# Performance work log

Measured on AMD Instinct MI355X. Metric: run time of the kernel, lower is better.

Reference implementation:

```python
import jax, jax.numpy as jnp
import numpy as np

HID = 2048      # hidden_size
H = 16          # num_heads == num_kv_heads (stack in fwd forces MHA)
DH = HID // H   # head_size = 128
QKV = 3 * H * DH  # 6144
THETA = 10000.0
EPS = 1e-5      # flash-attn RMSNorm default eps
B, L = 4, 2048


def setup_inputs() -> dict:
    key = jax.random.key(0)
    k1, k2, k3 = jax.random.split(key, 3)
    hidden_states = jax.random.normal(k1, (B, L, HID), dtype=jnp.float32)
    # weights stored as (in, out); scaled like a typical init so activations stay sane
    W_qkvg = jax.random.normal(k2, (HID, QKV + HID), dtype=jnp.float32) * 0.02
    W_out = jax.random.normal(k3, (HID, HID), dtype=jnp.float32) * 0.02
    return {"hidden_states": hidden_states, "W_qkvg": W_qkvg, "W_out": W_out}


def _rmsnorm(x):
    # elementwise_affine=False: pure rms normalization over head dim
    return x * jax.lax.rsqrt(jnp.mean(x * x, axis=-1, keepdims=True) + EPS)


def _rope(x, seqlen_offset=0):
    # x: (B, L, H, DH), non-interleaved (GPT-NeoX style rotate-half)
    half = DH // 2
    inv_freq = 1.0 / (THETA ** (jnp.arange(half, dtype=jnp.float32) * 2.0 / DH))
    pos = jnp.arange(seqlen_offset, seqlen_offset + x.shape[1], dtype=jnp.float32)
    ang = pos[:, None] * inv_freq[None, :]                  # (L, half)
    cos = jnp.cos(ang)[None, :, None, :]                    # (1,L,1,half)
    sin = jnp.sin(ang)[None, :, None, :]
    x1, x2 = x[..., :half], x[..., half:]
    return jnp.concatenate([x1 * cos - x2 * sin, x1 * sin + x2 * cos], axis=-1)


def _attention_forward(hidden_states, W_qkvg, W_out):
    b, l, _ = hidden_states.shape
    proj = hidden_states @ W_qkvg                           # (B,L,QKV+HID)
    qkv_flat, gate = proj[..., :QKV], proj[..., QKV:]
    gate = jax.nn.sigmoid(gate)
    qkv = qkv_flat.reshape(b, l, 3 * H, DH)
    q, k, v = qkv[:, :, :H], qkv[:, :, H:2 * H], qkv[:, :, 2 * H:]
    q = _rope(_rmsnorm(q))
    k = _rope(_rmsnorm(k))
    # causal softmax attention (math of flash_attn_func)
    scores = jnp.einsum('blhd,bmhd->bhlm', q, k) / np.sqrt(DH).astype(np.float32)
    causal = jnp.tril(jnp.ones((l, l), dtype=bool))
    scores = jnp.where(causal[None, None], scores, jnp.finfo(scores.dtype).min)
    attn = jax.nn.softmax(scores, axis=-1)
    out = jnp.einsum('bhlm,bmhd->blhd', attn, v).reshape(b, l, HID)
    out = out * gate
    return out @ W_out


def reference(hidden_states, W_qkvg, W_out):
    return _attention_forward(hidden_states, W_qkvg, W_out)
```

## Files before the change

### kernel.cpp

```cpp
#include <hip/hip_runtime.h>


typedef __attribute__((ext_vector_type(8))) short bf16x8;
typedef __attribute__((ext_vector_type(4))) float f32x4;
typedef __attribute__((ext_vector_type(4))) unsigned short us4;

#if __has_builtin(__builtin_amdgcn_exp2f)
#define EXP2(x) __builtin_amdgcn_exp2f(x)
#else
#define EXP2(x) exp2f(x)
#endif

__device__ __forceinline__ unsigned short f2bf(float f) {
    unsigned int x = __float_as_uint(f);
    unsigned int r = x + 0x7fffu + ((x >> 16) & 1u);
    return (unsigned short)(r >> 16);
}
__device__ __forceinline__ unsigned short f2bf_fast(float f) {
    return (unsigned short)((__float_as_uint(f) + 0x8000u) >> 16);
}
__device__ __forceinline__ float bf2f(unsigned short u) {
    return __uint_as_float(((unsigned int)u) << 16);
}

__device__ __forceinline__ void gll16(const unsigned short* g, unsigned short* l) {
    __builtin_amdgcn_global_load_lds(
        (const __attribute__((address_space(1))) unsigned int*)g,
        (__attribute__((address_space(3))) unsigned int*)l, 16, 0, 0);
}

__device__ __forceinline__ void barx() {
    asm volatile("" ::: "memory");
    __builtin_amdgcn_s_barrier();
    asm volatile("" ::: "memory");
}
#define LGKM0() asm volatile("s_waitcnt lgkmcnt(0)" ::: "memory")
#define VM6()   asm volatile("s_waitcnt vmcnt(6)" ::: "memory")
#define VM0()   asm volatile("s_waitcnt vmcnt(0)" ::: "memory")

__global__ __launch_bounds__(256) void cvt_bf16(const float* __restrict__ in,
                                                unsigned short* __restrict__ out) {
    int i = blockIdx.x * 256 + threadIdx.x;
    float4 v = ((const float4*)in)[i];
    us4 r;
    r[0] = f2bf(v.x); r[1] = f2bf(v.y); r[2] = f2bf(v.z); r[3] = f2bf(v.w);
    ((us4*)out)[i] = r;
}

__global__ __launch_bounds__(256) void transpose_cvt(const float* __restrict__ in,
                                                     unsigned short* __restrict__ out,
                                                     int R, int C) {
    __shared__ float t[32][33];
    int c0 = blockIdx.x * 32, r0 = blockIdx.y * 32;
    int tx = threadIdx.x, ty = threadIdx.y;
#pragma unroll
    for (int i = 0; i < 4; i++)
        t[ty + i * 8][tx] = in[(size_t)(r0 + ty + i * 8) * C + c0 + tx];
    __syncthreads();
#pragma unroll
    for (int i = 0; i < 4; i++)
        out[(size_t)(c0 + ty + i * 8) * R + r0 + tx] = f2bf(t[tx][ty + i * 8]);
}

__device__ __forceinline__ void gemm256_core(const unsigned short* __restrict__ A,
                                             const unsigned short* __restrict__ Bt,
                                             int K, int rowA0, int colB0,
                                             unsigned short* sm,
                                             f32x4 acc[8][4]) {
    const int tid = threadIdx.x;
    const int w = tid >> 6, lane = tid & 63;
    const int quad = lane >> 4, l15 = lane & 15;
    const int wm = w >> 2, wn = w & 3;
    const int lr = lane >> 3;
    const int lc = ((lane & 7) ^ lr) * 8;
    const int NT = K >> 6;

    const unsigned short* pA = A  + (size_t)(rowA0 + w * 16 + lr) * K + lc;
    const unsigned short* pB = Bt + (size_t)(colB0 + w * 16 + lr) * K + lc;
    unsigned short* lw = sm + w * 16 * 64;

#define STAGE(tt, isB, h)                                                       \
    do {                                                                        \
        const unsigned short* gp_ = ((isB) ? pB : pA) +                         \
            (size_t)(h) * 128 * K + (size_t)(tt) * 64;                          \
        unsigned short* lp_ = lw + (((tt) & 1) * 4 + (isB) * 2 + (h)) * 8192;   \
        gll16(gp_, lp_);                                                        \
        gll16(gp_ + (size_t)8 * K, lp_ + 8 * 64);                               \
    } while (0)

    STAGE(0, 1, 0); STAGE(0, 1, 1); STAGE(0, 0, 0); STAGE(0, 0, 1);
    STAGE(1, 1, 0); STAGE(1, 1, 1); STAGE(1, 0, 0);
    VM6();
    barx();

    for (int t = 0; t < NT; ++t) {
        const unsigned short* Asl = sm + ((t & 1) * 4 + wm) * 8192;
        const unsigned short* Bsl = sm + ((t & 1) * 4 + 2 + (wn >> 1)) * 8192;
        bf16x8 bfrag[4][2];
#pragma unroll
        for (int q = 0; q < 4; ++q) {
            if (q == 0) {
#pragma unroll
                for (int nj = 0; nj < 4; ++nj)
#pragma unroll
                    for (int kk = 0; kk < 2; ++kk) {
                        int r = (wn & 1) * 64 + nj * 16 + l15;
                        bfrag[nj][kk] = *(const bf16x8*)&Bsl[r * 64 +
                            (((kk * 4 + quad) ^ (r & 7)) * 8)];
                    }
            }
            bf16x8 afr[2][2];
#pragma unroll
            for (int mi = 0; mi < 2; ++mi)
#pragma unroll
                for (int kk = 0; kk < 2; ++kk) {
                    int r = q * 32 + mi * 16 + l15;
                    afr[mi][kk] = *(const bf16x8*)&Asl[r * 64 +
                        (((kk * 4 + quad) ^ (r & 7)) * 8)];
                }
            if (q == 0)      { if (t + 1 < NT) STAGE(t + 1, 0, 1); }
            else if (q == 1) { if (t + 2 < NT) STAGE(t + 2, 1, 0); }
            else if (q == 2) { if (t + 2 < NT) STAGE(t + 2, 1, 1); }
            else {
                if (t + 2 < NT)      { STAGE(t + 2, 0, 0); VM6(); }
                else if (t + 1 < NT) { VM0(); }
            }
            barx();
            LGKM0();
            __builtin_amdgcn_s_setprio(1);
#pragma unroll
            for (int mi = 0; mi < 2; ++mi)
#pragma unroll
                for (int nj = 0; nj < 4; ++nj)
#pragma unroll
                    for (int kk = 0; kk < 2; ++kk)
                        acc[q * 2 + mi][nj] = __builtin_amdgcn_mfma_f32_16x16x32_bf16(
                            afr[mi][kk], bfrag[nj][kk], acc[q * 2 + mi][nj], 0, 0, 0);
            __builtin_amdgcn_s_setprio(0);
            barx();
        }
    }
#undef STAGE
}

__global__ __launch_bounds__(512) void gemm_qkvg(const unsigned short* __restrict__ A,
                                                 const unsigned short* __restrict__ Bt,
                                                 unsigned short* __restrict__ Qb,
                                                 unsigned short* __restrict__ Kb,
                                                 unsigned short* __restrict__ Vt,
                                                 unsigned short* __restrict__ Gb) {
    __shared__ unsigned short sm[8 * 8192];
    f32x4 acc[8][4];
    f32x4 z = {0.f, 0.f, 0.f, 0.f};
#pragma unroll
    for (int i = 0; i < 8; i++)
#pragma unroll
        for (int j = 0; j < 4; j++) acc[i][j] = z;

    const int g = blockIdx.y * 32 + blockIdx.x;
    const int gs = (g & 7) * 128 + (g >> 3);
    const int bx = gs & 31, by = gs >> 5;
    const int rowA0 = by * 256, colB0 = bx * 256;
    gemm256_core(A, Bt, 2048, rowA0, colB0, sm, acc);

    const int tid = threadIdx.x, w = tid >> 6, lane = tid & 63;
    const int quad = lane >> 4, l15 = lane & 15;
    const int wm = w >> 2, wn = w & 3;
    const int sec = colB0 >> 11;
    const int hbase = (colB0 & 2047) >> 7;

    if (sec == 2) {
#pragma unroll
        for (int mi = 0; mi < 8; ++mi)
#pragma unroll
            for (int nj = 0; nj < 4; ++nj)
#pragma unroll
                for (int i = 0; i < 4; ++i) {
                    int ll = wm * 128 + mi * 16 + quad * 4 + i;
                    int c  = wn * 64 + nj * 16 + l15;
                    int hh = c >> 7, d = c & 127;
                    sm[hh * 32768 + d * 256 + (((ll >> 3) ^ (d & 31)) * 8) + (ll & 7)] =
                        f2bf(acc[mi][nj][i]);
                }
        __syncthreads();
        const int b_ = rowA0 >> 11, l0 = rowA0 & 2047;
        const int d = tid >> 2, part = tid & 3;
#pragma unroll
        for (int hh = 0; hh < 2; ++hh) {
            unsigned short* drow = Vt +
                ((size_t)(b_ * 16 + hbase + hh) * 128 + d) * 2048 + l0 + part * 64;
#pragma unroll
            for (int j = 0; j < 8; ++j) {
                int chunk = part * 8 + j;
                *(bf16x8*)(drow + j * 8) =
                    *(const bf16x8*)&sm[hh * 32768 + d * 256 + ((chunk ^ (d & 31)) * 8)];
            }
        }
    } else if (sec == 3) {
#pragma unroll
        for (int mi = 0; mi < 8; ++mi)
#pragma unroll
            for (int nj = 0; nj < 4; ++nj)
#pragma unroll
                for (int i = 0; i < 4; ++i) {
                    int rowg = rowA0 + wm * 128 + mi * 16 + quad * 4 + i;
                    int c = wn * 64 + nj * 16 + l15;
                    int h = hbase + (c >> 7), d = c & 127;
                    float gv = 1.f / (1.f + __expf(-acc[mi][nj][i]));
                    Gb[((size_t)rowg << 11) + h * 128 + d] = f2bf(gv);
                }
    } else {
        unsigned short* dst = (sec == 0) ? Qb : Kb;
#pragma unroll
        for (int mi = 0; mi < 8; ++mi)
#pragma unroll
            for (int nj = 0; nj < 4; ++nj)
#pragma unroll
                for (int i = 0; i < 4; ++i) {
                    int rowg = rowA0 + wm * 128 + mi * 16 + quad * 4 + i;
                    int c = wn * 64 + nj * 16 + l15;
                    int h = hbase + (c >> 7), d = c & 127;
                    int b_ = rowg >> 11, l_ = rowg & 2047;
                    dst[(((size_t)(b_ * 16 + h) * 2048 + l_) << 7) + d] =
                        f2bf(acc[mi][nj][i]);
                }
    }
}

__global__ __launch_bounds__(512) void gemm_out(const unsigned short* __restrict__ A,
                                                const unsigned short* __restrict__ Bt,
                                                float* __restrict__ C) {
    __shared__ unsigned short sm[8 * 8192];
    f32x4 acc[8][4];
    f32x4 z = {0.f, 0.f, 0.f, 0.f};
#pragma unroll
    for (int i = 0; i < 8; i++)
#pragma unroll
        for (int j = 0; j < 4; j++) acc[i][j] = z;

    const int g = blockIdx.y * 8 + blockIdx.x;
    const int gs = (g & 7) * 32 + (g >> 3);
    const int bx = gs & 7, by = gs >> 3;
    const int rowA0 = by * 256, colB0 = bx * 256;
    gemm256_core(A, Bt, 2048, rowA0, colB0, sm, acc);

    const int tid = threadIdx.x, w = tid >> 6, lane = tid & 63;
    const int quad = lane >> 4, l15 = lane & 15;
    const int wm = w >> 2, wn = w & 3;
#pragma unroll
    for (int mi = 0; mi < 8; ++mi)
#pragma unroll
        for (int nj = 0; nj < 4; ++nj)
#pragma unroll
            for (int i = 0; i < 4; ++i) {
                int rowg = rowA0 + wm * 128 + mi * 16 + quad * 4 + i;
                int col = colB0 + wn * 64 + nj * 16 + l15;
                C[(size_t)rowg * 2048 + col] = acc[mi][nj][i];
            }
}

__global__ __launch_bounds__(256) void rmsnorm_rope(unsigned short* __restrict__ Qp,
                                                    unsigned short* __restrict__ Kp) {
    unsigned short* X = blockIdx.y ? Kp : Qp;
    const int tid = threadIdx.x;
    const int row = blockIdx.x * 4 + (tid >> 6);
    const int lane = tid & 63;
    unsigned short* p = X + (size_t)row * 128;
    const int l_ = row & 2047;
    float x1 = bf2f(p[lane]);
    float x2 = bf2f(p[lane + 64]);
    float ss = x1 * x1 + x2 * x2;
#pragma unroll
    for (int off = 32; off >= 1; off >>= 1) ss += __shfl_xor(ss, off, 64);
    float r = rsqrtf(ss * (1.f / 128.f) + 1e-5f);
    x1 *= r; x2 *= r;
    float inv = exp2f(-(float)lane * (13.287712379549449f / 64.f));
    float ang = (float)l_ * inv;
    float sn, cs;
    sincosf(ang, &sn, &cs);
    p[lane]      = f2bf(x1 * cs - x2 * sn);
    p[lane + 64] = f2bf(x1 * sn + x2 * cs);
}

__global__ __launch_bounds__(512) void fa_kernel(const unsigned short* __restrict__ Q,
                                                 const unsigned short* __restrict__ K,
                                                 const unsigned short* __restrict__ Vt,
                                                 const unsigned short* __restrict__ G,
                                                 unsigned short* __restrict__ Og) {
    __shared__ unsigned short Ks[64 * 128];
    __shared__ unsigned short Vs[128 * 64];
    __shared__ unsigned short Ps[256 * 32];
    const int g = blockIdx.x;
    const int bh = (g & 7) | ((g >> 6) << 3);
    const int qc = (g >> 3) & 7;
    const int tid = threadIdx.x, w = tid >> 6, lane = tid & 63;
    const int quad = lane >> 4, l15 = lane & 15;
    const int sw = l15 & 7;
    const int qrow0 = qc * 256 + w * 32;
    const float CS = 0.12751740395609812f;

    bf16x8 qf[2][4];
#pragma unroll
    for (int mi = 0; mi < 2; mi++)
#pragma unroll
        for (int kt = 0; kt < 4; kt++)
            qf[mi][kt] = *(const bf16x8*)(Q + ((size_t)bh * 2048 + qrow0 + mi * 16 + l15) * 128
                                             + kt * 32 + quad * 8);

    f32x4 o[2][8];
    f32x4 z = {0.f, 0.f, 0.f, 0.f};
#pragma unroll
    for (int mi = 0; mi < 2; mi++)
#pragma unroll
        for (int nj = 0; nj < 8; nj++) o[mi][nj] = z;
    float rowsum[2][4];
#pragma unroll
    for (int mi = 0; mi < 2; mi++)
#pragma unroll
        for (int i = 0; i < 4; i++) rowsum[mi][i] = 0.f;

    const unsigned short* Kbase = K + (size_t)bh * 2048 * 128;
    const unsigned short* Vtb   = Vt + (size_t)bh * 128 * 2048;

    const int pr0 = w * 32 + l15, pr1 = pr0 + 16;
    const int pk0 = (pr0 >> 1) & 3, pk1 = (pr1 >> 1) & 3;

    const int NJ = 4 * (qc + 1);
    for (int j = 0; j < NJ; j++) {
        __syncthreads();

        {
            const int rowoff = lane >> 4, c = lane & 15;
#pragma unroll
            for (int i = 0; i < 2; i++) {
                int r0 = w * 8 + i * 4;
                int row = r0 + rowoff;
                int cs_ = (c & 8) | ((c & 7) ^ (row & 7));
                gll16(Kbase + (size_t)(j * 64 + row) * 128 + cs_ * 8, Ks + r0 * 128);
            }
        }
        {
            const int rowoff = lane >> 3, c = lane & 7;
#pragma unroll
            for (int i = 0; i < 2; i++) {
                int r0 = w * 16 + i * 8;
                int row = r0 + rowoff;
                gll16(Vtb + (size_t)row * 2048 + j * 64 + ((c ^ (row & 7)) * 8),
                      Vs + r0 * 64);
            }
        }
        __syncthreads();

        if (j * 64 >= qrow0 + 32) continue;

        f32x4 s[2][4];
#pragma unroll
        for (int mi = 0; mi < 2; mi++)
#pragma unroll
            for (int nj = 0; nj < 4; nj++) s[mi][nj] = z;
#pragma unroll
        for (int kt = 0; kt < 4; kt++)
#pragma unroll
            for (int nj = 0; nj < 4; nj++) {
                bf16x8 bfr = *(const bf16x8*)&Ks[(nj * 16 + l15) * 128 +
                                                 (((kt * 4 + quad) ^ sw) * 8)];
                s[0][nj] = __builtin_amdgcn_mfma_f32_16x16x32_bf16(qf[0][kt], bfr, s[0][nj], 0, 0, 0);
                s[1][nj] = __builtin_amdgcn_mfma_f32_16x16x32_bf16(qf[1][kt], bfr, s[1][nj], 0, 0, 0);
            }

        const bool diag = (j * 64 + 63 > qrow0);
#pragma unroll
        for (int hh = 0; hh < 2; hh++) {
#pragma unroll
            for (int mi = 0; mi < 2; mi++)
#pragma unroll
                for (int njh = 0; njh < 2; njh++) {
                    const int nj = hh * 2 + njh;
#pragma unroll
                    for (int i = 0; i < 4; i++) {
                        float pp = EXP2(s[mi][nj][i] * CS);
                        int row_l = mi * 16 + quad * 4 + i;
                        if (diag) {
                            int col_g = j * 64 + nj * 16 + l15;
                            if (col_g > qrow0 + row_l) pp = 0.f;
                        }
                        rowsum[mi][i] += pp;
                        int row = w * 32 + row_l;
                        int kv = njh * 16 + l15;
                        Ps[row * 32 + ((((kv >> 3) ^ ((row >> 1) & 3)) * 8)) + (kv & 7)] =
                            f2bf_fast(pp);
                    }
                }
            bf16x8 a0 = *(const bf16x8*)&Ps[pr0 * 32 + ((quad ^ pk0) * 8)];
            bf16x8 a1 = *(const bf16x8*)&Ps[pr1 * 32 + ((quad ^ pk1) * 8)];
#pragma unroll
            for (int nj = 0; nj < 8; nj++) {
                bf16x8 bfr = *(const bf16x8*)&Vs[(nj * 16 + l15) * 64 +
                                                 (((hh * 4 + quad) ^ sw) * 8)];
                o[0][nj] = __builtin_amdgcn_mfma_f32_16x16x32_bf16(a0, bfr, o[0][nj], 0, 0, 0);
                o[1][nj] = __builtin_amdgcn_mfma_f32_16x16x32_bf16(a1, bfr, o[1][nj], 0, 0, 0);
            }
        }
    }

    const int b_ = bh >> 4, h = bh & 15;
#pragma unroll
    for (int mi = 0; mi < 2; mi++)
#pragma unroll
        for (int i = 0; i < 4; i++) {
            float t = rowsum[mi][i];
#pragma unroll
            for (int off = 1; off < 16; off <<= 1) t += __shfl_xor(t, off, 16);
            float rl = 1.f / t;
            int l_ = qrow0 + mi * 16 + quad * 4 + i;
#pragma unroll
            for (int nj = 0; nj < 8; nj++) {
                int d = nj * 16 + l15;
                size_t gi = ((size_t)(b_ * 2048 + l_) * 2048) + h * 128 + d;
                Og[gi] = f2bf(o[mi][nj][i] * rl * bf2f(G[gi]));
            }
        }
}

extern "C" void kernel_launch(void* const* d_in, const int* in_sizes, int n_in,
                              void* d_out, int out_size, void* d_ws, size_t ws_size,
                              hipStream_t stream) {
    const float* X  = (const float*)d_in[0];
    const float* Wq = (const float*)d_in[1];
    const float* Wo = (const float*)d_in[2];
    float* out = (float*)d_out;

    char* ws = (char*)d_ws;
    const size_t SZ = 33554432ull;
    unsigned short* Xb  = (unsigned short*)(ws);
    unsigned short* Wqt = (unsigned short*)(ws + SZ);
    unsigned short* Wot = (unsigned short*)(ws + 2 * SZ);
    unsigned short* Qb  = (unsigned short*)(ws + 2 * SZ + 8388608ull);
    unsigned short* Kb  = (unsigned short*)(ws + 3 * SZ + 8388608ull);
    unsigned short* Vt  = (unsigned short*)(ws + 4 * SZ + 8388608ull);
    unsigned short* Gb  = (unsigned short*)(ws + 5 * SZ + 8388608ull);
    unsigned short* OG  = Xb;

    cvt_bf16<<<16384, 256, 0, stream>>>(X, Xb);
    transpose_cvt<<<dim3(256, 64), dim3(32, 8), 0, stream>>>(Wq, Wqt, 2048, 8192);
    transpose_cvt<<<dim3(64, 64),  dim3(32, 8), 0, stream>>>(Wo, Wot, 2048, 2048);

    gemm_qkvg<<<dim3(32, 32), 512, 0, stream>>>(Xb, Wqt, Qb, Kb, Vt, Gb);

    rmsnorm_rope<<<dim3(32768, 2), 256, 0, stream>>>(Qb, Kb);

    fa_kernel<<<512, 512, 0, stream>>>(Qb, Kb, Vt, Gb, OG);

    gemm_out<<<dim3(8, 32), 512, 0, stream>>>(OG, Wot, out);
}
```

Measured before the change: 702.7 us.

## Double-buffer K/V tiles in flash attention and remap QKVG GEMM block order

The attention kernel now keeps two LDS buffers for K and V. It issues the async global-to-LDS loads for the next tile before computing the current one, waiting with vmcnt(4) instead of a full drain, so load latency can overlap the MFMA and softmax work. Separately, the QKVG GEMM changes how block ids map to tiles: each XCD gets groups of four adjacent column tiles, which is meant to improve L2 reuse of B. The cost is double the K/V LDS footprint, which may reduce occupancy.

```diff
diff --git a/kernel.cpp b/kernel.cpp
--- a/kernel.cpp
+++ b/kernel.cpp
@@ -36,6 +36,7 @@
 }
 #define LGKM0() asm volatile("s_waitcnt lgkmcnt(0)" ::: "memory")
 #define VM6()   asm volatile("s_waitcnt vmcnt(6)" ::: "memory")
+#define VM4()   asm volatile("s_waitcnt vmcnt(4)" ::: "memory")
 #define VM0()   asm volatile("s_waitcnt vmcnt(0)" ::: "memory")
 
 __global__ __launch_bounds__(256) void cvt_bf16(const float* __restrict__ in,
@@ -158,8 +159,8 @@
         for (int j = 0; j < 4; j++) acc[i][j] = z;
 
     const int g = blockIdx.y * 32 + blockIdx.x;
-    const int gs = (g & 7) * 128 + (g >> 3);
-    const int bx = gs & 31, by = gs >> 5;
+    const int xcd = g & 7, lo = g >> 3;
+    const int bx = xcd * 4 + (lo & 3), by = lo >> 2;
     const int rowA0 = by * 256, colB0 = bx * 256;
     gemm256_core(A, Bt, 2048, rowA0, colB0, sm, acc);
 
@@ -287,8 +288,8 @@
                                                  const unsigned short* __restrict__ Vt,
                                                  const unsigned short* __restrict__ G,
                                                  unsigned short* __restrict__ Og) {
-    __shared__ unsigned short Ks[64 * 128];
-    __shared__ unsigned short Vs[128 * 64];
+    __shared__ unsigned short Ks[2][64 * 128];
+    __shared__ unsigned short Vs[2][128 * 64];
     __shared__ unsigned short Ps[256 * 32];
     const int g = blockIdx.x;
     const int bh = (g & 7) | ((g >> 6) << 3);
@@ -322,86 +323,94 @@
     const unsigned short* Kbase = K + (size_t)bh * 2048 * 128;
     const unsigned short* Vtb   = Vt + (size_t)bh * 128 * 2048;
 
+    const int krow = lane >> 4, kc = lane & 15;
+    const int vrow = lane >> 3, vc = lane & 7;
+
+#define STAGE_KV(jj, buf)                                                        \
+    do {                                                                         \
+        _Pragma("unroll")                                                        \
+        for (int i_ = 0; i_ < 2; i_++) {                                         \
+            int r0_ = w * 8 + i_ * 4;                                            \
+            int row_ = r0_ + krow;                                               \
+            int cs_ = (kc & 8) | ((kc & 7) ^ (row_ & 7));                        \
+            gll16(Kbase + (size_t)((jj) * 64 + row_) * 128 + cs_ * 8,            \
+                  &Ks[buf][r0_ * 128]);                                          \
+        }                                                                        \
+        _Pragma("unroll")                                                        \
+        for (int i_ = 0; i_ < 2; i_++) {                                         \
+            int r0_ = w * 16 + i_ * 8;                                           \
+            int row_ = r0_ + vrow;                                               \
+            gll16(Vtb + (size_t)row_ * 2048 + (jj) * 64 + ((vc ^ (row_ & 7)) * 8), \
+                  &Vs[buf][r0_ * 64]);                                           \
+        }                                                                        \
+    } while (0)
+
     const int pr0 = w * 32 + l15, pr1 = pr0 + 16;
     const int pk0 = (pr0 >> 1) & 3, pk1 = (pr1 >> 1) & 3;
 
     const int NJ = 4 * (qc + 1);
+
+    STAGE_KV(0, 0);
+
     for (int j = 0; j < NJ; j++) {
-        __syncthreads();
-
-        {
-            const int rowoff = lane >> 4, c = lane & 15;
-#pragma unroll
-            for (int i = 0; i < 2; i++) {
-                int r0 = w * 8 + i * 4;
-                int row = r0 + rowoff;
-                int cs_ = (c & 8) | ((c & 7) ^ (row & 7));
-                gll16(Kbase + (size_t)(j * 64 + row) * 128 + cs_ * 8, Ks + r0 * 128);
+        const int cur = j & 1;
+        if (j + 1 < NJ) { STAGE_KV(j + 1, cur ^ 1); VM4(); }
+        else            { VM0(); }
+        barx();
+
+        if (j * 64 < qrow0 + 32) {
+            f32x4 s[2][4];
+#pragma unroll
+            for (int mi = 0; mi < 2; mi++)
+#pragma unroll
+                for (int nj = 0; nj < 4; nj++) s[mi][nj] = z;
+#pragma unroll
+            for (int kt = 0; kt < 4; kt++)
+#pragma unroll
+                for (int nj = 0; nj < 4; nj++) {
+                    bf16x8 bfr = *(const bf16x8*)&Ks[cur][(nj * 16 + l15) * 128 +
+                                                         (((kt * 4 + quad) ^ sw) * 8)];
+                    s[0][nj] = __builtin_amdgcn_mfma_f32_16x16x32_bf16(qf[0][kt], bfr, s[0][nj], 0, 0, 0);
+                    s[1][nj] = __builtin_amdgcn_mfma_f32_16x16x32_bf16(qf[1][kt], bfr, s[1][nj], 0, 0, 0);
+                }
+
+            const bool diag = (j * 64 + 63 > qrow0);
+#pragma unroll
+            for (int hh = 0; hh < 2; hh++) {
+#pragma unroll
+                for (int mi = 0; mi < 2; mi++)
+#pragma unroll
+                    for (int njh = 0; njh < 2; njh++) {
+                        const int nj = hh * 2 + njh;
+#pragma unroll
+                        for (int i = 0; i < 4; i++) {
+                            float pp = EXP2(s[mi][nj][i] * CS);
+                            int row_l = mi * 16 + quad * 4 + i;
+                            if (diag) {
+                                int col_g = j * 64 + nj * 16 + l15;
+                                if (col_g > qrow0 + row_l) pp = 0.f;
+                            }
+                            rowsum[mi][i] += pp;
+                            int row = w * 32 + row_l;
+                            int kv = njh * 16 + l15;
+                            Ps[row * 32 + ((((kv >> 3) ^ ((row >> 1) & 3)) * 8)) + (kv & 7)] =
+                                f2bf_fast(pp);
+                        }
+                    }
+                bf16x8 a0 = *(const bf16x8*)&Ps[pr0 * 32 + ((quad ^ pk0) * 8)];
+                bf16x8 a1 = *(const bf16x8*)&Ps[pr1 * 32 + ((quad ^ pk1) * 8)];
+#pragma unroll
+                for (int nj = 0; nj < 8; nj++) {
+                    bf16x8 bfr = *(const bf16x8*)&Vs[cur][(nj * 16 + l15) * 64 +
+                                                          (((hh * 4 + quad) ^ sw) * 8)];
+                    o[0][nj] = __builtin_amdgcn_mfma_f32_16x16x32_bf16(a0, bfr, o[0][nj], 0, 0, 0);
+                    o[1][nj] = __builtin_amdgcn_mfma_f32_16x16x32_bf16(a1, bfr, o[1][nj], 0, 0, 0);
+                }
             }
         }
-        {
-            const int rowoff = lane >> 3, c = lane & 7;
-#pragma unroll
-            for (int i = 0; i < 2; i++) {
-                int r0 = w * 16 + i * 8;
-                int row = r0 + rowoff;
-                gll16(Vtb + (size_t)row * 2048 + j * 64 + ((c ^ (row & 7)) * 8),
-                      Vs + r0 * 64);
-            }
-        }
-        __syncthreads();
-
-        if (j * 64 >= qrow0 + 32) continue;
-
-        f32x4 s[2][4];
-#pragma unroll
-        for (int mi = 0; mi < 2; mi++)
-#pragma unroll
-            for (int nj = 0; nj < 4; nj++) s[mi][nj] = z;
-#pragma unroll
-        for (int kt = 0; kt < 4; kt++)
-#pragma unroll
-            for (int nj = 0; nj < 4; nj++) {
-                bf16x8 bfr = *(const bf16x8*)&Ks[(nj * 16 + l15) * 128 +
-                                                 (((kt * 4 + quad) ^ sw) * 8)];
-                s[0][nj] = __builtin_amdgcn_mfma_f32_16x16x32_bf16(qf[0][kt], bfr, s[0][nj], 0, 0, 0);
-                s[1][nj] = __builtin_amdgcn_mfma_f32_16x16x32_bf16(qf[1][kt], bfr, s[1][nj], 0, 0, 0);
-            }
-
-        const bool diag = (j * 64 + 63 > qrow0);
-#pragma unroll
-        for (int hh = 0; hh < 2; hh++) {
-#pragma unroll
-            for (int mi = 0; mi < 2; mi++)
-#pragma unroll
-                for (int njh = 0; njh < 2; njh++) {
-                    const int nj = hh * 2 + njh;
-#pragma unroll
-                    for (int i = 0; i < 4; i++) {
-                        float pp = EXP2(s[mi][nj][i] * CS);
-                        int row_l = mi * 16 + quad * 4 + i;
-                        if (diag) {
-                            int col_g = j * 64 + nj * 16 + l15;
-                            if (col_g > qrow0 + row_l) pp = 0.f;
-                        }
-                        rowsum[mi][i] += pp;
-                        int row = w * 32 + row_l;
-                        int kv = njh * 16 + l15;
-                        Ps[row * 32 + ((((kv >> 3) ^ ((row >> 1) & 3)) * 8)) + (kv & 7)] =
-                            f2bf_fast(pp);
-                    }
-                }
-            bf16x8 a0 = *(const bf16x8*)&Ps[pr0 * 32 + ((quad ^ pk0) * 8)];
-            bf16x8 a1 = *(const bf16x8*)&Ps[pr1 * 32 + ((quad ^ pk1) * 8)];
-#pragma unroll
-            for (int nj = 0; nj < 8; nj++) {
-                bf16x8 bfr = *(const bf16x8*)&Vs[(nj * 16 + l15) * 64 +
-                                                 (((hh * 4 + quad) ^ sw) * 8)];
-                o[0][nj] = __builtin_amdgcn_mfma_f32_16x16x32_bf16(a0, bfr, o[0][nj], 0, 0, 0);
-                o[1][nj] = __builtin_amdgcn_mfma_f32_16x16x32_bf16(a1, bfr, o[1][nj], 0, 0, 0);
-            }
-        }
+        barx();
     }
+#undef STAGE_KV
 
     const int b_ = bh >> 4, h = bh & 15;
 #pragma unroll
```

Result: no change. 715.6 us (+1.8%).
